# Kernel optimization log

Measured on AMD Instinct MI355X. Metric: run time of the kernel, lower is better.

## Reference

```python
import jax, jax.numpy as jnp
import numpy as np

D_MODEL = 768
NUM_HEADS = 12
D_K = D_MODEL // NUM_HEADS


def setup_inputs() -> dict:
    key = jax.random.key(0)
    ks = jax.random.split(key, 11)
    B, S = 2, 2048
    sc = 1.0 / np.sqrt(D_MODEL)
    return {
        "q": jax.random.normal(ks[0], (B, S, D_MODEL), jnp.float32),
        "k": jax.random.normal(ks[1], (B, S, D_MODEL), jnp.float32),
        "v": jax.random.normal(ks[2], (B, S, D_MODEL), jnp.float32),
        "w_q": jax.random.normal(ks[3], (D_MODEL, D_MODEL), jnp.float32) * sc,
        "b_q": jnp.zeros((D_MODEL,), jnp.float32),
        "w_k": jax.random.normal(ks[4], (D_MODEL, D_MODEL), jnp.float32) * sc,
        "b_k": jnp.zeros((D_MODEL,), jnp.float32),
        "w_v": jax.random.normal(ks[5], (D_MODEL, D_MODEL), jnp.float32) * sc,
        "b_v": jnp.zeros((D_MODEL,), jnp.float32),
        "w_o": jax.random.normal(ks[6], (D_MODEL, D_MODEL), jnp.float32) * sc,
        "b_o": jnp.zeros((D_MODEL,), jnp.float32),
    }


def _split_heads(x, B):
    # [B, S, D] -> [B, H, S, d_k]
    return x.reshape(B, -1, NUM_HEADS, D_K).transpose(0, 2, 1, 3)


def reference(q, k, v, w_q, b_q, w_k, b_k, w_v, b_v, w_o, b_o):
    B = q.shape[0]
    # torch nn.Linear: y = x @ W.T + b; weights stored [out, in]
    qh = _split_heads(q @ w_q.T + b_q, B)
    kh = _split_heads(k @ w_k.T + b_k, B)
    vh = _split_heads(v @ w_v.T + b_v, B)
    scores = jnp.einsum("bhsd,bhtd->bhst", qh, kh) / jnp.sqrt(jnp.float32(D_K))
    attn = jax.nn.softmax(scores, axis=-1)
    ctx = jnp.einsum("bhst,bhtd->bhsd", attn, vh)
    ctx = ctx.transpose(0, 2, 1, 3).reshape(B, -1, D_MODEL)
    return ctx @ w_o.T + b_o
```

## Files before the change

### kernel.cpp

```cpp
#include <hip/hip_runtime.h>
#include <cstdint>


#define S_LEN 2048
#define NHEAD 12
#define DMODEL 768

typedef short s16x8 __attribute__((ext_vector_type(8)));
typedef float f32x4 __attribute__((ext_vector_type(4)));
typedef float f32x16 __attribute__((ext_vector_type(16)));

#define MFMA16(a, b, c) __builtin_amdgcn_mfma_f32_16x16x32_bf16((a), (b), (c), 0, 0, 0)
#define MFMA32(a, b, c) __builtin_amdgcn_mfma_f32_32x32x16_bf16((a), (b), (c), 0, 0, 0)

__device__ __forceinline__ void lds_dma16(void* lds, const void* g) {
  __builtin_amdgcn_global_load_lds(
      (const __attribute__((address_space(1))) unsigned int*)g,
      (__attribute__((address_space(3))) unsigned int*)lds, 16, 0, 0);
}

__device__ __forceinline__ unsigned int pk_bf16(float a, float b) {
  unsigned int ua = __float_as_uint(a), ub = __float_as_uint(b);
  ua = (ua + 0x7FFFu + ((ua >> 16) & 1u)) >> 16;
  ub = (ub + 0x7FFFu + ((ub >> 16) & 1u)) >> 16;
  return ua | (ub << 16);
}
__device__ __forceinline__ short bf16r(float a) {
  unsigned int ua = __float_as_uint(a);
  return (short)((ua + 0x7FFFu + ((ua >> 16) & 1u)) >> 16);
}
__device__ __forceinline__ unsigned int pk_trunc(float a, float b) {
  return __builtin_amdgcn_perm(__float_as_uint(b), __float_as_uint(a), 0x07060302u);
}
__device__ __forceinline__ float bf16_floor(float a) {
  return __uint_as_float(__float_as_uint(a) & 0xFFFF0000u);
}

__global__ __launch_bounds__(256)
void convert_all(const float* __restrict__ q, const float* __restrict__ k,
                 const float* __restrict__ v,
                 const float* __restrict__ w0, const float* __restrict__ w1,
                 const float* __restrict__ w2, const float* __restrict__ w3,
                 short* __restrict__ qb, short* __restrict__ kb,
                 short* __restrict__ vb,
                 short* __restrict__ o0, short* __restrict__ o1,
                 short* __restrict__ o2, short* __restrict__ o3) {
  int b = blockIdx.x;
  const float* src;
  short* dst;
  if (b < 9216) {
    const int s = b / 3072;
    src = (s == 0) ? q : (s == 1) ? k : v;
    dst = (s == 0) ? qb : (s == 1) ? kb : vb;
    b -= s * 3072;
  } else {
    b -= 9216;
    const int s = b / 576;
    src = (s == 0) ? w0 : (s == 1) ? w1 : (s == 2) ? w2 : w3;
    dst = (s == 0) ? o0 : (s == 1) ? o1 : (s == 2) ? o2 : o3;
    b -= s * 576;
  }
  const long i = ((long)b * 256 + threadIdx.x) * 4;
  float4 f = *(const float4*)(src + i);
  uint2 u;
  u.x = pk_bf16(f.x, f.y);
  u.y = pk_bf16(f.z, f.w);
  *(uint2*)(dst + i) = u;
}

__global__ __launch_bounds__(256)
void qkv_kernel(const short* __restrict__ qb, const short* __restrict__ kb,
                const short* __restrict__ vb,
                const short* __restrict__ wq, const short* __restrict__ wk,
                const short* __restrict__ wv,
                const float* __restrict__ bq, const float* __restrict__ bk,
                const float* __restrict__ bv,
                short* __restrict__ qh, short* __restrict__ kh,
                short* __restrict__ vt) {
  constexpr int K = 768;
  __shared__ short Abuf[128 * 32];
  __shared__ short Bbuf[128 * 32];

  const int L   = blockIdx.x;
  const int xcd = L & 7;
  const int i   = L >> 3;
  const int nt  = i % 6;
  const int pl  = xcd * 12 + i / 6;
  const int z   = pl >> 5;
  const int mt  = pl & 31;
  const int m0  = mt * 128;
  const int n0  = nt * 128;

  const short* A = (z == 0) ? qb : (z == 1) ? kb : vb;
  const short* B = (z == 0) ? wq : (z == 1) ? wk : wv;
  const float* bias = (z == 0) ? bq : (z == 1) ? bk : bv;

  const int tid  = threadIdx.x;
  const int lane = tid & 63;
  const int w    = tid >> 6;
  const int g    = lane >> 4;
  const int c    = lane & 15;
  const int wm   = (w & 1) * 64;
  const int wn   = (w >> 1) * 64;

  const int drow = w * 32 + (lane >> 2);
  const int dcol = (lane & 3) * 8;
  const short* Ag = A + (long)(m0 + drow) * K + dcol;
  const short* Bg = B + (long)(n0 + drow) * K + dcol;
  short* Al0 = &Abuf[w * 1024];
  short* Al1 = &Abuf[w * 1024 + 512];
  short* Bl0 = &Bbuf[w * 1024];
  short* Bl1 = &Bbuf[w * 1024 + 512];

  f32x4 acc[4][4];
#pragma unroll
  for (int a = 0; a < 4; ++a)
#pragma unroll
    for (int b2 = 0; b2 < 4; ++b2) acc[a][b2] = (f32x4){0.f, 0.f, 0.f, 0.f};

  for (int kt = 0; kt < K; kt += 32) {
    lds_dma16(Al0, Ag + kt);
    lds_dma16(Al1, Ag + (long)16 * K + kt);
    lds_dma16(Bl0, Bg + kt);
    lds_dma16(Bl1, Bg + (long)16 * K + kt);
    __syncthreads();

    s16x8 af[4], bf[4];
#pragma unroll
    for (int mb = 0; mb < 4; ++mb)
      af[mb] = *(const s16x8*)&Abuf[(wm + mb * 16 + c) * 32 + g * 8];
#pragma unroll
    for (int nb = 0; nb < 4; ++nb)
      bf[nb] = *(const s16x8*)&Bbuf[(wn + nb * 16 + c) * 32 + g * 8];
#pragma unroll
    for (int mb = 0; mb < 4; ++mb)
#pragma unroll
      for (int nb = 0; nb < 4; ++nb)
        acc[mb][nb] = MFMA16(af[mb], bf[nb], acc[mb][nb]);
    __syncthreads();
  }

  if (z < 2) {
    short* outp = z ? kh : qh;
    const float scale = z ? 1.0f : 0.18033688011112042f;
#pragma unroll
    for (int mb = 0; mb < 4; ++mb) {
#pragma unroll
      for (int nb = 0; nb < 4; ++nb) {
        const int n = n0 + wn + nb * 16 + c;
        const float bvv = bias[n];
        const int hh = n >> 6, d = n & 63;
#pragma unroll
        for (int r = 0; r < 4; ++r) {
          const int m = m0 + wm + mb * 16 + g * 4 + r;
          const int b2 = m >> 11, s = m & 2047;
          const float val = (acc[mb][nb][r] + bvv) * scale;
          outp[(((long)(b2 * NHEAD + hh) * S_LEN + s) << 6) + d] = bf16r(val);
        }
      }
    }
  } else {
#pragma unroll
    for (int mb = 0; mb < 4; ++mb) {
#pragma unroll
      for (int nb = 0; nb < 4; ++nb) {
        const int n = n0 + wn + nb * 16 + c;
        const float bvv = bias[n];
        const int hh = n >> 6, d = n & 63;
        const int m_base = m0 + wm + mb * 16 + g * 4;
        const int b2 = m_base >> 11, t = m_base & 2047;
        uint2 ov;
        ov.x = pk_bf16(acc[mb][nb][0] + bvv, acc[mb][nb][1] + bvv);
        ov.y = pk_bf16(acc[mb][nb][2] + bvv, acc[mb][nb][3] + bvv);
        *(uint2*)(vt + ((long)(b2 * NHEAD + hh) * 64 + d) * S_LEN + t) = ov;
      }
    }
  }
}

__global__ __launch_bounds__(256)
void o_kernel(const short* __restrict__ ctx, const short* __restrict__ wo,
              const float* __restrict__ bo, float* __restrict__ out) {
  constexpr int K = 768;
  __shared__ short Abuf[64 * 32];
  __shared__ short Bbuf[128 * 32];

  const int L   = blockIdx.x;
  const int xcd = L & 7;
  const int i   = L >> 3;
  const int nt  = i % 6;
  const int mt  = xcd * 8 + i / 6;
  const int m0  = mt * 64;
  const int n0  = nt * 128;

  const int tid  = threadIdx.x;
  const int lane = tid & 63;
  const int w    = tid >> 6;
  const int g    = lane >> 4;
  const int c    = lane & 15;
  const int wm   = (w & 1) * 32;
  const int wn   = (w >> 1) * 64;

  const int arow = w * 16 + (lane >> 2);
  const int brow = w * 32 + (lane >> 2);
  const int dcol = (lane & 3) * 8;
  const short* Ag = ctx + (long)(m0 + arow) * K + dcol;
  const short* Bg = wo + (long)(n0 + brow) * K + dcol;
  short* Al = &Abuf[w * 512];
  short* Bl0 = &Bbuf[w * 1024];
  short* Bl1 = &Bbuf[w * 1024 + 512];

  f32x4 acc[2][4];
#pragma unroll
  for (int a = 0; a < 2; ++a)
#pragma unroll
    for (int b2 = 0; b2 < 4; ++b2) acc[a][b2] = (f32x4){0.f, 0.f, 0.f, 0.f};

  for (int kt = 0; kt < K; kt += 32) {
    lds_dma16(Al, Ag + kt);
    lds_dma16(Bl0, Bg + kt);
    lds_dma16(Bl1, Bg + (long)16 * K + kt);
    __syncthreads();

    s16x8 af[2], bf[4];
#pragma unroll
    for (int mb = 0; mb < 2; ++mb)
      af[mb] = *(const s16x8*)&Abuf[(wm + mb * 16 + c) * 32 + g * 8];
#pragma unroll
    for (int nb = 0; nb < 4; ++nb)
      bf[nb] = *(const s16x8*)&Bbuf[(wn + nb * 16 + c) * 32 + g * 8];
#pragma unroll
    for (int mb = 0; mb < 2; ++mb)
#pragma unroll
      for (int nb = 0; nb < 4; ++nb)
        acc[mb][nb] = MFMA16(af[mb], bf[nb], acc[mb][nb]);
    __syncthreads();
  }

#pragma unroll
  for (int mb = 0; mb < 2; ++mb) {
#pragma unroll
    for (int nb = 0; nb < 4; ++nb) {
      const int n = n0 + wn + nb * 16 + c;
      const float bvv = bo[n];
#pragma unroll
      for (int r = 0; r < 4; ++r) {
        const int m = m0 + wm + mb * 16 + g * 4 + r;
        out[(long)m * DMODEL + n] = acc[mb][nb][r] + bvv;
      }
    }
  }
}

__global__ __launch_bounds__(256, 3)
void attn_kernel(const short* __restrict__ Qh, const short* __restrict__ Kh,
                 const short* __restrict__ Vt, short* __restrict__ Ctx) {
  __shared__ short kbuf[2][64 * 64];
  __shared__ short vbuf[2][64 * 64];

  const int tid  = threadIdx.x;
  const int lane = tid & 63;
  const int w    = tid >> 6;
  const int par  = w & 1;
  const int rh   = w >> 1;
  const int q32  = lane & 31;
  const int hi   = lane >> 5;
  const int bh   = blockIdx.y;
  const int qs0  = blockIdx.x * 64;
  const long base = (long)bh * S_LEN * 64;
  const short* Qb = Qh + base;
  const short* Kb = Kh + base;
  const short* Vb = Vt + base;

  const long qrow = (long)(qs0 + rh * 32 + q32) * 64;
  s16x8 qf[4];
#pragma unroll
  for (int db = 0; db < 4; ++db)
    qf[db] = *(const s16x8*)(Qb + qrow + db * 16 + hi * 8);

  f32x16 co0, co1;
#pragma unroll
  for (int i = 0; i < 16; ++i) { co0[i] = 0.f; co1[i] = 0.f; }
  float l_lane = 0.f;

  const int srow = tid >> 2;
  const int sq   = tid & 3;
  const int sw   = srow & 7;
  const int sg0  = ((2 * sq)     ^ sw) * 8;
  const int sg1  = ((2 * sq + 1) ^ sw) * 8;
  const short* kg = Kb + (long)srow * 64 + sq * 16;
  const short* vg = Vb + (long)srow * S_LEN + sq * 16;

  uint4 rkE0, rkE1, rvE0, rvE1, rkO0, rkO1, rvO0, rvO1;
  auto fetch_pair = [&](long tE, long tO) {
    rkE0 = *(const uint4*)(kg + tE * 64);
    rkE1 = *(const uint4*)(kg + tE * 64 + 8);
    rvE0 = *(const uint4*)(vg + tE);
    rvE1 = *(const uint4*)(vg + tE + 8);
    rkO0 = *(const uint4*)(kg + tO * 64);
    rkO1 = *(const uint4*)(kg + tO * 64 + 8);
    rvO0 = *(const uint4*)(vg + tO);
    rvO1 = *(const uint4*)(vg + tO + 8);
  };
  auto store_pair = [&]() {
    *(uint4*)&kbuf[0][srow * 64 + sg0] = rkE0;
    *(uint4*)&kbuf[0][srow * 64 + sg1] = rkE1;
    *(uint4*)&vbuf[0][srow * 64 + sg0] = rvE0;
    *(uint4*)&vbuf[0][srow * 64 + sg1] = rvE1;
    *(uint4*)&kbuf[1][srow * 64 + sg0] = rkO0;
    *(uint4*)&kbuf[1][srow * 64 + sg1] = rkO1;
    *(uint4*)&vbuf[1][srow * 64 + sg0] = rvO0;
    *(uint4*)&vbuf[1][srow * 64 + sg1] = rvO1;
  };

  const int tw = lane & 7;
  int c4[4];
#pragma unroll
  for (int i = 0; i < 4; ++i) c4[i] = ((2 * i + hi) ^ tw) * 8;
  const int row0 = q32 * 64;
  const int row1 = (32 + q32) * 64;
  const short* kb2 = kbuf[par];
  const short* vb2 = vbuf[par];

  auto mkfrag = [&](unsigned a, unsigned b, unsigned c, unsigned d) -> s16x8 {
    asm("v_permlane32_swap_b32 %0, %1" : "+v"(a), "+v"(c));
    asm("v_permlane32_swap_b32 %0, %1" : "+v"(b), "+v"(d));
    uint4 u;
    u.x = a; u.y = b; u.z = c; u.w = d;
    return __builtin_bit_cast(s16x8, u);
  };

  auto step = [&]() {
    f32x16 s0, s1;
#pragma unroll
    for (int i = 0; i < 16; ++i) { s0[i] = 0.f; s1[i] = 0.f; }
    __builtin_amdgcn_s_setprio(1);
#pragma unroll
    for (int db = 0; db < 4; ++db) {
      const s16x8 k0 = *(const s16x8*)&kb2[row0 + c4[db]];
      const s16x8 k1 = *(const s16x8*)&kb2[row1 + c4[db]];
      s0 = MFMA32(k0, qf[db], s0);
      s1 = MFMA32(k1, qf[db], s1);
    }
    __builtin_amdgcn_s_setprio(0);
    unsigned pk0[8], pk1[8];
#pragma unroll
    for (int i = 0; i < 8; ++i) {
      float a0 = __builtin_amdgcn_exp2f(s0[2 * i]);
      float b0 = __builtin_amdgcn_exp2f(s0[2 * i + 1]);
      float a1 = __builtin_amdgcn_exp2f(s1[2 * i]);
      float b1 = __builtin_amdgcn_exp2f(s1[2 * i + 1]);
      l_lane += (bf16_floor(a0) + bf16_floor(b0)) +
                (bf16_floor(a1) + bf16_floor(b1));
      pk0[i] = pk_trunc(a0, b0);
      pk1[i] = pk_trunc(a1, b1);
    }
    s16x8 pf0 = mkfrag(pk0[0], pk0[1], pk0[2], pk0[3]);
    s16x8 pf1 = mkfrag(pk0[4], pk0[5], pk0[6], pk0[7]);
    s16x8 pf2 = mkfrag(pk1[0], pk1[1], pk1[2], pk1[3]);
    s16x8 pf3 = mkfrag(pk1[4], pk1[5], pk1[6], pk1[7]);
    __builtin_amdgcn_s_setprio(1);
#pragma unroll
    for (int sl = 0; sl < 4; ++sl) {
      const s16x8 v0 = *(const s16x8*)&vb2[row0 + c4[sl]];
      const s16x8 v1 = *(const s16x8*)&vb2[row1 + c4[sl]];
      const s16x8 pf = (sl == 0) ? pf0 : (sl == 1) ? pf1 : (sl == 2) ? pf2 : pf3;
      co0 = MFMA32(v0, pf, co0);
      co1 = MFMA32(v1, pf, co1);
    }
    __builtin_amdgcn_s_setprio(0);
  };

  constexpr int NT = S_LEN / 64;
  fetch_pair(0, 64);
  store_pair();
  for (int ph = 0; ph < NT / 2; ++ph) {
    __syncthreads();
    const long tE = (2 * ph + 2 < NT) ? (long)(2 * ph + 2) * 64 : 0;
    const long tO = (2 * ph + 3 < NT) ? (long)(2 * ph + 3) * 64 : 0;
    fetch_pair(tE, tO);
    step();
    __syncthreads();
    store_pair();
  }

  float rs = l_lane + __shfl_xor(l_lane, 32);

  __syncthreads();
  float* mbuf = (float*)((rh == 0) ? (short*)kbuf : (short*)vbuf);
  float* mp = mbuf + lane * 36;
  if (par) {
#pragma unroll
    for (int i = 0; i < 4; ++i) {
      *(float4*)(mp + 4 * i)      = make_float4(co0[4*i], co0[4*i+1], co0[4*i+2], co0[4*i+3]);
      *(float4*)(mp + 16 + 4 * i) = make_float4(co1[4*i], co1[4*i+1], co1[4*i+2], co1[4*i+3]);
    }
    mp[32] = rs;
  }
  __syncthreads();
  if (!par) {
#pragma unroll
    for (int i = 0; i < 4; ++i) {
      float4 a = *(const float4*)(mp + 4 * i);
      float4 b = *(const float4*)(mp + 16 + 4 * i);
      co0[4*i] += a.x; co0[4*i+1] += a.y; co0[4*i+2] += a.z; co0[4*i+3] += a.w;
      co1[4*i] += b.x; co1[4*i+1] += b.y; co1[4*i+2] += b.z; co1[4*i+3] += b.w;
    }
    rs += mp[32];
    const float invl = 1.f / rs;

    const int hh = bh % NHEAD;
    const long tok = (long)(bh / NHEAD) * S_LEN + qs0 + rh * 32 + q32;
    short* outp = Ctx + tok * DMODEL + hh * 64;
#pragma unroll
    for (int rq = 0; rq < 4; ++rq) {
      const int d0 = 8 * rq + 4 * hi;
      uint2 ov;
      ov.x = pk_bf16(co0[4*rq] * invl, co0[4*rq+1] * invl);
      ov.y = pk_bf16(co0[4*rq+2] * invl, co0[4*rq+3] * invl);
      *(uint2*)(outp + d0) = ov;
      uint2 ov2;
      ov2.x = pk_bf16(co1[4*rq] * invl, co1[4*rq+1] * invl);
      ov2.y = pk_bf16(co1[4*rq+2] * invl, co1[4*rq+3] * invl);
      *(uint2*)(outp + 32 + d0) = ov2;
    }
  }
}

extern "C" void kernel_launch(void* const* d_in, const int* in_sizes, int n_in,
                              void* d_out, int out_size, void* d_ws, size_t ws_size,
                              hipStream_t stream) {
  const float* q   = (const float*)d_in[0];
  const float* k   = (const float*)d_in[1];
  const float* v   = (const float*)d_in[2];
  const float* w_q = (const float*)d_in[3];
  const float* b_q = (const float*)d_in[4];
  const float* w_k = (const float*)d_in[5];
  const float* b_k = (const float*)d_in[6];
  const float* w_v = (const float*)d_in[7];
  const float* b_v = (const float*)d_in[8];
  const float* w_o = (const float*)d_in[9];
  const float* b_o = (const float*)d_in[10];
  float* out = (float*)d_out;

  const long NELEM = (long)2 * NHEAD * S_LEN * 64;
  const long WELEM = (long)DMODEL * DMODEL;
  short* qh  = (short*)d_ws;
  short* kh  = qh + NELEM;
  short* vt  = kh + NELEM;
  short* wqb = vt + NELEM;
  short* wkb = wqb + WELEM;
  short* wvb = wkb + WELEM;
  short* wob = wvb + WELEM;
  short* qb  = wob + WELEM;
  short* kb  = qb + NELEM;
  short* vb  = kb + NELEM;
  short* ctx = qb;

  dim3 blk(256);
  convert_all<<<dim3(11520), blk, 0, stream>>>(q, k, v, w_q, w_k, w_v, w_o,
                                               qb, kb, vb, wqb, wkb, wvb, wob);
  qkv_kernel<<<dim3(576), blk, 0, stream>>>(qb, kb, vb, wqb, wkb, wvb,
                                            b_q, b_k, b_v, qh, kh, vt);
  attn_kernel<<<dim3(32, 24), blk, 0, stream>>>(qh, kh, vt, ctx);
  o_kernel<<<dim3(384), blk, 0, stream>>>(ctx, wob, b_o, out);
}
```

Measured before the change: 193.1 us.

## Load V fragments directly from global into registers, dropping V shared-memory staging

V tiles are no longer staged through LDS. Each wave now loads its MFMA V operands straight from global memory into registers, prefetching the next tile after the PV MFMAs. This removes the LDS stores and reads for V and frees LDS, which may help occupancy. In exchange, global loads are issued per wave without sharing between the two row-half waves, so L2 traffic and register pressure go up and load latency is exposed. The row-sum accumulation is also split into two partial sums to shorten the dependency chain.

```diff
diff --git a/kernel.cpp b/kernel.cpp
--- a/kernel.cpp
+++ b/kernel.cpp
@@ -256,7 +256,7 @@
 void attn_kernel(const short* __restrict__ Qh, const short* __restrict__ Kh,
                  const short* __restrict__ Vt, short* __restrict__ Ctx) {
   __shared__ short kbuf[2][64 * 64];
-  __shared__ short vbuf[2][64 * 64];
+  __shared__ float mbuf[2][64 * 36];
 
   const int tid  = threadIdx.x;
   const int lane = tid & 63;
@@ -289,28 +289,30 @@
   const int sg0  = ((2 * sq)     ^ sw) * 8;
   const int sg1  = ((2 * sq + 1) ^ sw) * 8;
   const short* kg = Kb + (long)srow * 64 + sq * 16;
-  const short* vg = Vb + (long)srow * S_LEN + sq * 16;
-
-  uint4 rkE0, rkE1, rvE0, rvE1, rkO0, rkO1, rvO0, rvO1;
+
+  uint4 rkE0, rkE1, rkO0, rkO1;
   auto fetch_pair = [&](long tE, long tO) {
     rkE0 = *(const uint4*)(kg + tE * 64);
     rkE1 = *(const uint4*)(kg + tE * 64 + 8);
-    rvE0 = *(const uint4*)(vg + tE);
-    rvE1 = *(const uint4*)(vg + tE + 8);
     rkO0 = *(const uint4*)(kg + tO * 64);
     rkO1 = *(const uint4*)(kg + tO * 64 + 8);
-    rvO0 = *(const uint4*)(vg + tO);
-    rvO1 = *(const uint4*)(vg + tO + 8);
   };
   auto store_pair = [&]() {
     *(uint4*)&kbuf[0][srow * 64 + sg0] = rkE0;
     *(uint4*)&kbuf[0][srow * 64 + sg1] = rkE1;
-    *(uint4*)&vbuf[0][srow * 64 + sg0] = rvE0;
-    *(uint4*)&vbuf[0][srow * 64 + sg1] = rvE1;
     *(uint4*)&kbuf[1][srow * 64 + sg0] = rkO0;
     *(uint4*)&kbuf[1][srow * 64 + sg1] = rkO1;
-    *(uint4*)&vbuf[1][srow * 64 + sg0] = rvO0;
-    *(uint4*)&vbuf[1][srow * 64 + sg1] = rvO1;
+  };
+
+  const short* vrow0 = Vb + (long)q32 * S_LEN + hi * 8;
+  const short* vrow1 = vrow0 + (long)32 * S_LEN;
+  s16x8 vf0[4], vf1[4];
+  auto vload = [&](long t0) {
+#pragma unroll
+    for (int sl = 0; sl < 4; ++sl) {
+      vf0[sl] = *(const s16x8*)(vrow0 + t0 + sl * 16);
+      vf1[sl] = *(const s16x8*)(vrow1 + t0 + sl * 16);
+    }
   };
 
   const int tw = lane & 7;
@@ -320,7 +322,6 @@
   const int row0 = q32 * 64;
   const int row1 = (32 + q32) * 64;
   const short* kb2 = kbuf[par];
-  const short* vb2 = vbuf[par];
 
   auto mkfrag = [&](unsigned a, unsigned b, unsigned c, unsigned d) -> s16x8 {
     asm("v_permlane32_swap_b32 %0, %1" : "+v"(a), "+v"(c));
@@ -330,7 +331,7 @@
     return __builtin_bit_cast(s16x8, u);
   };
 
-  auto step = [&]() {
+  auto step = [&](long tv_next) {
     f32x16 s0, s1;
 #pragma unroll
     for (int i = 0; i < 16; ++i) { s0[i] = 0.f; s1[i] = 0.f; }
@@ -344,42 +345,47 @@
     }
     __builtin_amdgcn_s_setprio(0);
     unsigned pk0[8], pk1[8];
+    float la = 0.f, lb = 0.f;
 #pragma unroll
     for (int i = 0; i < 8; ++i) {
       float a0 = __builtin_amdgcn_exp2f(s0[2 * i]);
       float b0 = __builtin_amdgcn_exp2f(s0[2 * i + 1]);
       float a1 = __builtin_amdgcn_exp2f(s1[2 * i]);
       float b1 = __builtin_amdgcn_exp2f(s1[2 * i + 1]);
-      l_lane += (bf16_floor(a0) + bf16_floor(b0)) +
-                (bf16_floor(a1) + bf16_floor(b1));
+      la += bf16_floor(a0) + bf16_floor(b0);
+      lb += bf16_floor(a1) + bf16_floor(b1);
       pk0[i] = pk_trunc(a0, b0);
       pk1[i] = pk_trunc(a1, b1);
     }
+    l_lane += la + lb;
     s16x8 pf0 = mkfrag(pk0[0], pk0[1], pk0[2], pk0[3]);
     s16x8 pf1 = mkfrag(pk0[4], pk0[5], pk0[6], pk0[7]);
     s16x8 pf2 = mkfrag(pk1[0], pk1[1], pk1[2], pk1[3]);
     s16x8 pf3 = mkfrag(pk1[4], pk1[5], pk1[6], pk1[7]);
     __builtin_amdgcn_s_setprio(1);
-#pragma unroll
-    for (int sl = 0; sl < 4; ++sl) {
-      const s16x8 v0 = *(const s16x8*)&vb2[row0 + c4[sl]];
-      const s16x8 v1 = *(const s16x8*)&vb2[row1 + c4[sl]];
-      const s16x8 pf = (sl == 0) ? pf0 : (sl == 1) ? pf1 : (sl == 2) ? pf2 : pf3;
-      co0 = MFMA32(v0, pf, co0);
-      co1 = MFMA32(v1, pf, co1);
-    }
+    co0 = MFMA32(vf0[0], pf0, co0);
+    co1 = MFMA32(vf1[0], pf0, co1);
+    co0 = MFMA32(vf0[1], pf1, co0);
+    co1 = MFMA32(vf1[1], pf1, co1);
+    co0 = MFMA32(vf0[2], pf2, co0);
+    co1 = MFMA32(vf1[2], pf2, co1);
+    co0 = MFMA32(vf0[3], pf3, co0);
+    co1 = MFMA32(vf1[3], pf3, co1);
     __builtin_amdgcn_s_setprio(0);
+    vload(tv_next);
   };
 
   constexpr int NT = S_LEN / 64;
   fetch_pair(0, 64);
   store_pair();
+  vload((long)par * 64);
   for (int ph = 0; ph < NT / 2; ++ph) {
     __syncthreads();
     const long tE = (2 * ph + 2 < NT) ? (long)(2 * ph + 2) * 64 : 0;
     const long tO = (2 * ph + 3 < NT) ? (long)(2 * ph + 3) * 64 : 0;
     fetch_pair(tE, tO);
-    step();
+    const long tv = (2 * ph + 2 + par < NT) ? (long)(2 * ph + 2 + par) * 64 : 0;
+    step(tv);
     __syncthreads();
     store_pair();
   }
@@ -387,8 +393,7 @@
   float rs = l_lane + __shfl_xor(l_lane, 32);
 
   __syncthreads();
-  float* mbuf = (float*)((rh == 0) ? (short*)kbuf : (short*)vbuf);
-  float* mp = mbuf + lane * 36;
+  float* mp = mbuf[rh] + lane * 36;
   if (par) {
 #pragma unroll
     for (int i = 0; i < 4; ++i) {
```

Result: slower. 213.0 us (+10.3%).

## Give each wave private K/V tiles and all 64 queries, dropping block barriers

Applied to the files above, without the earlier changes.

The attention kernel now splits the key sequence across the four waves. Each wave loads its own 64-key K/V tile into a private LDS slice and processes all 64 query rows against it, reusing each K/V fragment for two query groups. This removes the per-tile __syncthreads and the shared staging, and the next tile's global loads overlap with compute. The cost is more registers (four accumulators plus staged loads), lower occupancy (launch bound 3→2), 64 KB of LDS, and a larger 4-way cross-wave reduction at the end.

```diff
diff --git a/kernel.cpp b/kernel.cpp
--- a/kernel.cpp
+++ b/kernel.cpp
@@ -252,17 +252,14 @@
   }
 }
 
-__global__ __launch_bounds__(256, 3)
+__global__ __launch_bounds__(256, 2)
 void attn_kernel(const short* __restrict__ Qh, const short* __restrict__ Kh,
                  const short* __restrict__ Vt, short* __restrict__ Ctx) {
-  __shared__ short kbuf[2][64 * 64];
-  __shared__ short vbuf[2][64 * 64];
+  __shared__ short sbuf[32768];
 
   const int tid  = threadIdx.x;
   const int lane = tid & 63;
   const int w    = tid >> 6;
-  const int par  = w & 1;
-  const int rh   = w >> 1;
   const int q32  = lane & 31;
   const int hi   = lane >> 5;
   const int bh   = blockIdx.y;
@@ -272,45 +269,50 @@
   const short* Kb = Kh + base;
   const short* Vb = Vt + base;
 
-  const long qrow = (long)(qs0 + rh * 32 + q32) * 64;
-  s16x8 qf[4];
-#pragma unroll
-  for (int db = 0; db < 4; ++db)
-    qf[db] = *(const s16x8*)(Qb + qrow + db * 16 + hi * 8);
-
-  f32x16 co0, co1;
-#pragma unroll
-  for (int i = 0; i < 16; ++i) { co0[i] = 0.f; co1[i] = 0.f; }
-  float l_lane = 0.f;
-
-  const int srow = tid >> 2;
-  const int sq   = tid & 3;
-  const int sw   = srow & 7;
-  const int sg0  = ((2 * sq)     ^ sw) * 8;
-  const int sg1  = ((2 * sq + 1) ^ sw) * 8;
-  const short* kg = Kb + (long)srow * 64 + sq * 16;
-  const short* vg = Vb + (long)srow * S_LEN + sq * 16;
-
-  uint4 rkE0, rkE1, rvE0, rvE1, rkO0, rkO1, rvO0, rvO1;
-  auto fetch_pair = [&](long tE, long tO) {
-    rkE0 = *(const uint4*)(kg + tE * 64);
-    rkE1 = *(const uint4*)(kg + tE * 64 + 8);
-    rvE0 = *(const uint4*)(vg + tE);
-    rvE1 = *(const uint4*)(vg + tE + 8);
-    rkO0 = *(const uint4*)(kg + tO * 64);
-    rkO1 = *(const uint4*)(kg + tO * 64 + 8);
-    rvO0 = *(const uint4*)(vg + tO);
-    rvO1 = *(const uint4*)(vg + tO + 8);
+  short* klds = sbuf + w * 8192;
+  short* vlds = klds + 4096;
+
+  s16x8 qfA[4], qfB[4];
+  {
+    const long qrA = (long)(qs0 + q32) * 64;
+    const long qrB = (long)(qs0 + 32 + q32) * 64;
+#pragma unroll
+    for (int db = 0; db < 4; ++db) {
+      qfA[db] = *(const s16x8*)(Qb + qrA + db * 16 + hi * 8);
+      qfB[db] = *(const s16x8*)(Qb + qrB + db * 16 + hi * 8);
+    }
+  }
+
+  f32x16 co00, co01, co10, co11;
+#pragma unroll
+  for (int i = 0; i < 16; ++i) {
+    co00[i] = 0.f; co01[i] = 0.f; co10[i] = 0.f; co11[i] = 0.f;
+  }
+  float l0 = 0.f, l1 = 0.f;
+
+  const int srw = lane >> 3;
+  const int sc  = lane & 7;
+  const int swz = (sc ^ srw) * 8;
+  const short* kgb = Kb + (long)srw * 64 + sc * 8;
+  const short* vgb = Vb + (long)srw * S_LEN + sc * 8;
+
+  uint4 kst[8], vst[8];
+  auto fetchK = [&](long t0) {
+#pragma unroll
+    for (int i = 0; i < 8; ++i)
+      kst[i] = *(const uint4*)(kgb + (t0 + i * 8) * 64);
   };
-  auto store_pair = [&]() {
-    *(uint4*)&kbuf[0][srow * 64 + sg0] = rkE0;
-    *(uint4*)&kbuf[0][srow * 64 + sg1] = rkE1;
-    *(uint4*)&vbuf[0][srow * 64 + sg0] = rvE0;
-    *(uint4*)&vbuf[0][srow * 64 + sg1] = rvE1;
-    *(uint4*)&kbuf[1][srow * 64 + sg0] = rkO0;
-    *(uint4*)&kbuf[1][srow * 64 + sg1] = rkO1;
-    *(uint4*)&vbuf[1][srow * 64 + sg0] = rvO0;
-    *(uint4*)&vbuf[1][srow * 64 + sg1] = rvO1;
+  auto fetchV = [&](long t0) {
+#pragma unroll
+    for (int i = 0; i < 8; ++i)
+      vst[i] = *(const uint4*)(vgb + (long)i * 8 * S_LEN + t0);
+  };
+  auto lwrite = [&]() {
+#pragma unroll
+    for (int i = 0; i < 8; ++i) {
+      *(uint4*)&klds[(i * 8 + srw) * 64 + swz] = kst[i];
+      *(uint4*)&vlds[(i * 8 + srw) * 64 + swz] = vst[i];
+    }
   };
 
   const int tw = lane & 7;
@@ -319,8 +321,6 @@
   for (int i = 0; i < 4; ++i) c4[i] = ((2 * i + hi) ^ tw) * 8;
   const int row0 = q32 * 64;
   const int row1 = (32 + q32) * 64;
-  const short* kb2 = kbuf[par];
-  const short* vb2 = vbuf[par];
 
   auto mkfrag = [&](unsigned a, unsigned b, unsigned c, unsigned d) -> s16x8 {
     asm("v_permlane32_swap_b32 %0, %1" : "+v"(a), "+v"(c));
@@ -330,99 +330,140 @@
     return __builtin_bit_cast(s16x8, u);
   };
 
-  auto step = [&]() {
-    f32x16 s0, s1;
-#pragma unroll
-    for (int i = 0; i < 16; ++i) { s0[i] = 0.f; s1[i] = 0.f; }
+  constexpr int NT = S_LEN / 64;
+  fetchK((long)w * 64);
+  fetchV((long)w * 64);
+  lwrite();
+  asm volatile("s_waitcnt lgkmcnt(0)" ::: "memory");
+
+  for (int jt = w; jt < NT; jt += 4) {
+    const int nx = jt + 4;
+    const bool pre = (nx < NT);
+    if (pre) fetchK((long)nx * 64);
+
+    f32x16 s00, s01, s10, s11;
+#pragma unroll
+    for (int i = 0; i < 16; ++i) {
+      s00[i] = 0.f; s01[i] = 0.f; s10[i] = 0.f; s11[i] = 0.f;
+    }
     __builtin_amdgcn_s_setprio(1);
 #pragma unroll
     for (int db = 0; db < 4; ++db) {
-      const s16x8 k0 = *(const s16x8*)&kb2[row0 + c4[db]];
-      const s16x8 k1 = *(const s16x8*)&kb2[row1 + c4[db]];
-      s0 = MFMA32(k0, qf[db], s0);
-      s1 = MFMA32(k1, qf[db], s1);
+      const s16x8 k0 = *(const s16x8*)&klds[row0 + c4[db]];
+      const s16x8 k1 = *(const s16x8*)&klds[row1 + c4[db]];
+      s00 = MFMA32(k0, qfA[db], s00);
+      s10 = MFMA32(k0, qfB[db], s10);
+      s01 = MFMA32(k1, qfA[db], s01);
+      s11 = MFMA32(k1, qfB[db], s11);
     }
     __builtin_amdgcn_s_setprio(0);
-    unsigned pk0[8], pk1[8];
+
+    if (pre) fetchV((long)nx * 64);
+
+    unsigned pA0[8], pA1[8], pB0[8], pB1[8];
 #pragma unroll
     for (int i = 0; i < 8; ++i) {
-      float a0 = __builtin_amdgcn_exp2f(s0[2 * i]);
-      float b0 = __builtin_amdgcn_exp2f(s0[2 * i + 1]);
-      float a1 = __builtin_amdgcn_exp2f(s1[2 * i]);
-      float b1 = __builtin_amdgcn_exp2f(s1[2 * i + 1]);
-      l_lane += (bf16_floor(a0) + bf16_floor(b0)) +
-                (bf16_floor(a1) + bf16_floor(b1));
-      pk0[i] = pk_trunc(a0, b0);
-      pk1[i] = pk_trunc(a1, b1);
-    }
-    s16x8 pf0 = mkfrag(pk0[0], pk0[1], pk0[2], pk0[3]);
-    s16x8 pf1 = mkfrag(pk0[4], pk0[5], pk0[6], pk0[7]);
-    s16x8 pf2 = mkfrag(pk1[0], pk1[1], pk1[2], pk1[3]);
-    s16x8 pf3 = mkfrag(pk1[4], pk1[5], pk1[6], pk1[7]);
+      float xa = __builtin_amdgcn_exp2f(s00[2 * i]);
+      float xb = __builtin_amdgcn_exp2f(s00[2 * i + 1]);
+      float ya = __builtin_amdgcn_exp2f(s01[2 * i]);
+      float yb = __builtin_amdgcn_exp2f(s01[2 * i + 1]);
+      l0 += (bf16_floor(xa) + bf16_floor(xb)) + (bf16_floor(ya) + bf16_floor(yb));
+      pA0[i] = pk_trunc(xa, xb);
+      pA1[i] = pk_trunc(ya, yb);
+      float za = __builtin_amdgcn_exp2f(s10[2 * i]);
+      float zb = __builtin_amdgcn_exp2f(s10[2 * i + 1]);
+      float wa = __builtin_amdgcn_exp2f(s11[2 * i]);
+      float wb = __builtin_amdgcn_exp2f(s11[2 * i + 1]);
+      l1 += (bf16_floor(za) + bf16_floor(zb)) + (bf16_floor(wa) + bf16_floor(wb));
+      pB0[i] = pk_trunc(za, zb);
+      pB1[i] = pk_trunc(wa, wb);
+    }
+    s16x8 pfA[4], pfB[4];
+    pfA[0] = mkfrag(pA0[0], pA0[1], pA0[2], pA0[3]);
+    pfA[1] = mkfrag(pA0[4], pA0[5], pA0[6], pA0[7]);
+    pfA[2] = mkfrag(pA1[0], pA1[1], pA1[2], pA1[3]);
+    pfA[3] = mkfrag(pA1[4], pA1[5], pA1[6], pA1[7]);
+    pfB[0] = mkfrag(pB0[0], pB0[1], pB0[2], pB0[3]);
+    pfB[1] = mkfrag(pB0[4], pB0[5], pB0[6], pB0[7]);
+    pfB[2] = mkfrag(pB1[0], pB1[1], pB1[2], pB1[3]);
+    pfB[3] = mkfrag(pB1[4], pB1[5], pB1[6], pB1[7]);
+
     __builtin_amdgcn_s_setprio(1);
 #pragma unroll
     for (int sl = 0; sl < 4; ++sl) {
-      const s16x8 v0 = *(const s16x8*)&vb2[row0 + c4[sl]];
-      const s16x8 v1 = *(const s16x8*)&vb2[row1 + c4[sl]];
-      const s16x8 pf = (sl == 0) ? pf0 : (sl == 1) ? pf1 : (sl == 2) ? pf2 : pf3;
-      co0 = MFMA32(v0, pf, co0);
-      co1 = MFMA32(v1, pf, co1);
+      const s16x8 v0 = *(const s16x8*)&vlds[row0 + c4[sl]];
+      const s16x8 v1 = *(const s16x8*)&vlds[row1 + c4[sl]];
+      co00 = MFMA32(v0, pfA[sl], co00);
+      co10 = MFMA32(v0, pfB[sl], co10);
+      co01 = MFMA32(v1, pfA[sl], co01);
+      co11 = MFMA32(v1, pfB[sl], co11);
     }
     __builtin_amdgcn_s_setprio(0);
-  };
-
-  constexpr int NT = S_LEN / 64;
-  fetch_pair(0, 64);
-  store_pair();
-  for (int ph = 0; ph < NT / 2; ++ph) {
-    __syncthreads();
-    const long tE = (2 * ph + 2 < NT) ? (long)(2 * ph + 2) * 64 : 0;
-    const long tO = (2 * ph + 3 < NT) ? (long)(2 * ph + 3) * 64 : 0;
-    fetch_pair(tE, tO);
-    step();
-    __syncthreads();
-    store_pair();
-  }
-
-  float rs = l_lane + __shfl_xor(l_lane, 32);
+
+    if (pre) {
+      lwrite();
+      asm volatile("s_waitcnt lgkmcnt(0)" ::: "memory");
+    }
+  }
+
+  float rs0 = l0 + __shfl_xor(l0, 32);
+  float rs1 = l1 + __shfl_xor(l1, 32);
 
   __syncthreads();
-  float* mbuf = (float*)((rh == 0) ? (short*)kbuf : (short*)vbuf);
-  float* mp = mbuf + lane * 36;
-  if (par) {
+  float* M = (float*)sbuf;
+  if (w > 0) {
+    float* mp = M + ((w - 1) * 64 + lane) * 68;
 #pragma unroll
     for (int i = 0; i < 4; ++i) {
-      *(float4*)(mp + 4 * i)      = make_float4(co0[4*i], co0[4*i+1], co0[4*i+2], co0[4*i+3]);
-      *(float4*)(mp + 16 + 4 * i) = make_float4(co1[4*i], co1[4*i+1], co1[4*i+2], co1[4*i+3]);
-    }
-    mp[32] = rs;
+      *(float4*)(mp + 4 * i)      = make_float4(co00[4*i], co00[4*i+1], co00[4*i+2], co00[4*i+3]);
+      *(float4*)(mp + 16 + 4 * i) = make_float4(co01[4*i], co01[4*i+1], co01[4*i+2], co01[4*i+3]);
+      *(float4*)(mp + 32 + 4 * i) = make_float4(co10[4*i], co10[4*i+1], co10[4*i+2], co10[4*i+3]);
+      *(float4*)(mp + 48 + 4 * i) = make_float4(co11[4*i], co11[4*i+1], co11[4*i+2], co11[4*i+3]);
+    }
+    mp[64] = rs0;
+    mp[65] = rs1;
   }
   __syncthreads();
-  if (!par) {
-#pragma unroll
-    for (int i = 0; i < 4; ++i) {
-      float4 a = *(const float4*)(mp + 4 * i);
-      float4 b = *(const float4*)(mp + 16 + 4 * i);
-      co0[4*i] += a.x; co0[4*i+1] += a.y; co0[4*i+2] += a.z; co0[4*i+3] += a.w;
-      co1[4*i] += b.x; co1[4*i+1] += b.y; co1[4*i+2] += b.z; co1[4*i+3] += b.w;
-    }
-    rs += mp[32];
-    const float invl = 1.f / rs;
+  if (w == 0) {
+    for (int sw = 0; sw < 3; ++sw) {
+      const float* mp = M + (sw * 64 + lane) * 68;
+#pragma unroll
+      for (int i = 0; i < 4; ++i) {
+        float4 x0 = *(const float4*)(mp + 4 * i);
+        float4 x1 = *(const float4*)(mp + 16 + 4 * i);
+        float4 x2 = *(const float4*)(mp + 32 + 4 * i);
+        float4 x3 = *(const float4*)(mp + 48 + 4 * i);
+        co00[4*i] += x0.x; co00[4*i+1] += x0.y; co00[4*i+2] += x0.z; co00[4*i+3] += x0.w;
+        co01[4*i] += x1.x; co01[4*i+1] += x1.y; co01[4*i+2] += x1.z; co01[4*i+3] += x1.w;
+        co10[4*i] += x2.x; co10[4*i+1] += x2.y; co10[4*i+2] += x2.z; co10[4*i+3] += x2.w;
+        co11[4*i] += x3.x; co11[4*i+1] += x3.y; co11[4*i+2] += x3.z; co11[4*i+3] += x3.w;
+      }
+      rs0 += mp[64];
+      rs1 += mp[65];
+    }
+    const float inv0 = 1.f / rs0;
+    const float inv1 = 1.f / rs1;
 
     const int hh = bh % NHEAD;
-    const long tok = (long)(bh / NHEAD) * S_LEN + qs0 + rh * 32 + q32;
-    short* outp = Ctx + tok * DMODEL + hh * 64;
+    const long tokA = (long)(bh / NHEAD) * S_LEN + qs0 + q32;
+    short* opA = Ctx + tokA * DMODEL + hh * 64;
+    short* opB = opA + (long)32 * DMODEL;
 #pragma unroll
     for (int rq = 0; rq < 4; ++rq) {
       const int d0 = 8 * rq + 4 * hi;
       uint2 ov;
-      ov.x = pk_bf16(co0[4*rq] * invl, co0[4*rq+1] * invl);
-      ov.y = pk_bf16(co0[4*rq+2] * invl, co0[4*rq+3] * invl);
-      *(uint2*)(outp + d0) = ov;
-      uint2 ov2;
-      ov2.x = pk_bf16(co1[4*rq] * invl, co1[4*rq+1] * invl);
-      ov2.y = pk_bf16(co1[4*rq+2] * invl, co1[4*rq+3] * invl);
-      *(uint2*)(outp + 32 + d0) = ov2;
+      ov.x = pk_bf16(co00[4*rq] * inv0, co00[4*rq+1] * inv0);
+      ov.y = pk_bf16(co00[4*rq+2] * inv0, co00[4*rq+3] * inv0);
+      *(uint2*)(opA + d0) = ov;
+      ov.x = pk_bf16(co01[4*rq] * inv0, co01[4*rq+1] * inv0);
+      ov.y = pk_bf16(co01[4*rq+2] * inv0, co01[4*rq+3] * inv0);
+      *(uint2*)(opA + 32 + d0) = ov;
+      ov.x = pk_bf16(co10[4*rq] * inv1, co10[4*rq+1] * inv1);
+      ov.y = pk_bf16(co10[4*rq+2] * inv1, co10[4*rq+3] * inv1);
+      *(uint2*)(opB + d0) = ov;
+      ov.x = pk_bf16(co11[4*rq] * inv1, co11[4*rq+1] * inv1);
+      ov.y = pk_bf16(co11[4*rq+2] * inv1, co11[4*rq+3] * inv1);
+      *(uint2*)(opB + 32 + d0) = ov;
     }
   }
 }
```

Result: slower. 270.1 us (+39.9%).

## Double K-tile depth to 64 with XOR-swizzled LDS in projection GEMMs

Applied to the files above, without the earlier changes.

The QKV and output projection GEMMs now stage 64-wide K slices per iteration instead of 32, which halves the number of barrier pairs per tile. The LDS layout uses an XOR swizzle of 16-byte chunks by row, with precomputed fragment offsets, to avoid bank conflicts on the wider rows. The attention step also splits the row-sum accumulation into two independent partial sums to shorten the dependency chain. The cost is doubled LDS use per block, which could reduce occupancy.

```diff
diff --git a/kernel.cpp b/kernel.cpp
--- a/kernel.cpp
+++ b/kernel.cpp
@@ -78,8 +78,8 @@
                 short* __restrict__ qh, short* __restrict__ kh,
                 short* __restrict__ vt) {
   constexpr int K = 768;
-  __shared__ short Abuf[128 * 32];
-  __shared__ short Bbuf[128 * 32];
+  __shared__ short Abuf[128 * 64];
+  __shared__ short Bbuf[128 * 64];
 
   const int L   = blockIdx.x;
   const int xcd = L & 7;
@@ -103,14 +103,12 @@
   const int wm   = (w & 1) * 64;
   const int wn   = (w >> 1) * 64;
 
-  const int drow = w * 32 + (lane >> 2);
-  const int dcol = (lane & 3) * 8;
-  const short* Ag = A + (long)(m0 + drow) * K + dcol;
-  const short* Bg = B + (long)(n0 + drow) * K + dcol;
-  short* Al0 = &Abuf[w * 1024];
-  short* Al1 = &Abuf[w * 1024 + 512];
-  short* Bl0 = &Bbuf[w * 1024];
-  short* Bl1 = &Bbuf[w * 1024 + 512];
+  const int lr   = lane >> 3;
+  const int dchk = ((lane & 7) ^ lr) * 8;
+  const short* Ag = A + (long)(m0 + w * 32 + lr) * K + dchk;
+  const short* Bg = B + (long)(n0 + w * 32 + lr) * K + dchk;
+  short* Al = &Abuf[(w * 32) * 64];
+  short* Bl = &Bbuf[(w * 32) * 64];
 
   f32x4 acc[4][4];
 #pragma unroll
@@ -118,25 +116,40 @@
 #pragma unroll
     for (int b2 = 0; b2 < 4; ++b2) acc[a][b2] = (f32x4){0.f, 0.f, 0.f, 0.f};
 
-  for (int kt = 0; kt < K; kt += 32) {
-    lds_dma16(Al0, Ag + kt);
-    lds_dma16(Al1, Ag + (long)16 * K + kt);
-    lds_dma16(Bl0, Bg + kt);
-    lds_dma16(Bl1, Bg + (long)16 * K + kt);
+  int aoff[4][2], boff[4][2];
+#pragma unroll
+  for (int mb = 0; mb < 4; ++mb)
+#pragma unroll
+    for (int kk = 0; kk < 2; ++kk) {
+      const int Ra = wm + mb * 16 + c;
+      const int Rb = wn + mb * 16 + c;
+      aoff[mb][kk] = Ra * 64 + (((kk * 4 + g) ^ (Ra & 7)) * 8);
+      boff[mb][kk] = Rb * 64 + (((kk * 4 + g) ^ (Rb & 7)) * 8);
+    }
+
+  for (int kt = 0; kt < K; kt += 64) {
+#pragma unroll
+    for (int ii = 0; ii < 4; ++ii) {
+      lds_dma16(Al + ii * 8 * 64, Ag + (long)ii * 8 * K + kt);
+      lds_dma16(Bl + ii * 8 * 64, Bg + (long)ii * 8 * K + kt);
+    }
     __syncthreads();
 
-    s16x8 af[4], bf[4];
-#pragma unroll
-    for (int mb = 0; mb < 4; ++mb)
-      af[mb] = *(const s16x8*)&Abuf[(wm + mb * 16 + c) * 32 + g * 8];
-#pragma unroll
-    for (int nb = 0; nb < 4; ++nb)
-      bf[nb] = *(const s16x8*)&Bbuf[(wn + nb * 16 + c) * 32 + g * 8];
-#pragma unroll
-    for (int mb = 0; mb < 4; ++mb)
+#pragma unroll
+    for (int kk = 0; kk < 2; ++kk) {
+      s16x8 af[4], bf[4];
+#pragma unroll
+      for (int mb = 0; mb < 4; ++mb)
+        af[mb] = *(const s16x8*)&Abuf[aoff[mb][kk]];
 #pragma unroll
       for (int nb = 0; nb < 4; ++nb)
-        acc[mb][nb] = MFMA16(af[mb], bf[nb], acc[mb][nb]);
+        bf[nb] = *(const s16x8*)&Bbuf[boff[nb][kk]];
+#pragma unroll
+      for (int mb = 0; mb < 4; ++mb)
+#pragma unroll
+        for (int nb = 0; nb < 4; ++nb)
+          acc[mb][nb] = MFMA16(af[mb], bf[nb], acc[mb][nb]);
+    }
     __syncthreads();
   }
 
@@ -182,8 +195,8 @@
 void o_kernel(const short* __restrict__ ctx, const short* __restrict__ wo,
               const float* __restrict__ bo, float* __restrict__ out) {
   constexpr int K = 768;
-  __shared__ short Abuf[64 * 32];
-  __shared__ short Bbuf[128 * 32];
+  __shared__ short Abuf[64 * 64];
+  __shared__ short Bbuf[128 * 64];
 
   const int L   = blockIdx.x;
   const int xcd = L & 7;
@@ -201,14 +214,12 @@
   const int wm   = (w & 1) * 32;
   const int wn   = (w >> 1) * 64;
 
-  const int arow = w * 16 + (lane >> 2);
-  const int brow = w * 32 + (lane >> 2);
-  const int dcol = (lane & 3) * 8;
-  const short* Ag = ctx + (long)(m0 + arow) * K + dcol;
-  const short* Bg = wo + (long)(n0 + brow) * K + dcol;
-  short* Al = &Abuf[w * 512];
-  short* Bl0 = &Bbuf[w * 1024];
-  short* Bl1 = &Bbuf[w * 1024 + 512];
+  const int lr   = lane >> 3;
+  const int dchk = ((lane & 7) ^ lr) * 8;
+  const short* Ag = ctx + (long)(m0 + w * 16 + lr) * K + dchk;
+  const short* Bg = wo + (long)(n0 + w * 32 + lr) * K + dchk;
+  short* Al = &Abuf[(w * 16) * 64];
+  short* Bl = &Bbuf[(w * 32) * 64];
 
   f32x4 acc[2][4];
 #pragma unroll
@@ -216,24 +227,45 @@
 #pragma unroll
     for (int b2 = 0; b2 < 4; ++b2) acc[a][b2] = (f32x4){0.f, 0.f, 0.f, 0.f};
 
-  for (int kt = 0; kt < K; kt += 32) {
-    lds_dma16(Al, Ag + kt);
-    lds_dma16(Bl0, Bg + kt);
-    lds_dma16(Bl1, Bg + (long)16 * K + kt);
+  int aoff[2][2], boff[4][2];
+#pragma unroll
+  for (int kk = 0; kk < 2; ++kk) {
+#pragma unroll
+    for (int mb = 0; mb < 2; ++mb) {
+      const int Ra = wm + mb * 16 + c;
+      aoff[mb][kk] = Ra * 64 + (((kk * 4 + g) ^ (Ra & 7)) * 8);
+    }
+#pragma unroll
+    for (int nb = 0; nb < 4; ++nb) {
+      const int Rb = wn + nb * 16 + c;
+      boff[nb][kk] = Rb * 64 + (((kk * 4 + g) ^ (Rb & 7)) * 8);
+    }
+  }
+
+  for (int kt = 0; kt < K; kt += 64) {
+#pragma unroll
+    for (int ii = 0; ii < 2; ++ii)
+      lds_dma16(Al + ii * 8 * 64, Ag + (long)ii * 8 * K + kt);
+#pragma unroll
+    for (int ii = 0; ii < 4; ++ii)
+      lds_dma16(Bl + ii * 8 * 64, Bg + (long)ii * 8 * K + kt);
     __syncthreads();
 
-    s16x8 af[2], bf[4];
-#pragma unroll
-    for (int mb = 0; mb < 2; ++mb)
-      af[mb] = *(const s16x8*)&Abuf[(wm + mb * 16 + c) * 32 + g * 8];
-#pragma unroll
-    for (int nb = 0; nb < 4; ++nb)
-      bf[nb] = *(const s16x8*)&Bbuf[(wn + nb * 16 + c) * 32 + g * 8];
-#pragma unroll
-    for (int mb = 0; mb < 2; ++mb)
+#pragma unroll
+    for (int kk = 0; kk < 2; ++kk) {
+      s16x8 af[2], bf[4];
+#pragma unroll
+      for (int mb = 0; mb < 2; ++mb)
+        af[mb] = *(const s16x8*)&Abuf[aoff[mb][kk]];
 #pragma unroll
       for (int nb = 0; nb < 4; ++nb)
-        acc[mb][nb] = MFMA16(af[mb], bf[nb], acc[mb][nb]);
+        bf[nb] = *(const s16x8*)&Bbuf[boff[nb][kk]];
+#pragma unroll
+      for (int mb = 0; mb < 2; ++mb)
+#pragma unroll
+        for (int nb = 0; nb < 4; ++nb)
+          acc[mb][nb] = MFMA16(af[mb], bf[nb], acc[mb][nb]);
+    }
     __syncthreads();
   }
 
@@ -344,17 +376,19 @@
     }
     __builtin_amdgcn_s_setprio(0);
     unsigned pk0[8], pk1[8];
+    float la = 0.f, lb = 0.f;
 #pragma unroll
     for (int i = 0; i < 8; ++i) {
       float a0 = __builtin_amdgcn_exp2f(s0[2 * i]);
       float b0 = __builtin_amdgcn_exp2f(s0[2 * i + 1]);
       float a1 = __builtin_amdgcn_exp2f(s1[2 * i]);
       float b1 = __builtin_amdgcn_exp2f(s1[2 * i + 1]);
-      l_lane += (bf16_floor(a0) + bf16_floor(b0)) +
-                (bf16_floor(a1) + bf16_floor(b1));
+      la += bf16_floor(a0) + bf16_floor(b0);
+      lb += bf16_floor(a1) + bf16_floor(b1);
       pk0[i] = pk_trunc(a0, b0);
       pk1[i] = pk_trunc(a1, b1);
     }
+    l_lane += la + lb;
     s16x8 pf0 = mkfrag(pk0[0], pk0[1], pk0[2], pk0[3]);
     s16x8 pf1 = mkfrag(pk0[4], pk0[5], pk0[6], pk0[7]);
     s16x8 pf2 = mkfrag(pk1[0], pk1[1], pk1[2], pk1[3]);
```

Result: faster. 187.8 us, median of 2 (-2.7%).
